# Kernel tuning notes

Hardware: AMD Instinct MI355X
Metric: run time of the kernel (lower is better)

## Reference

```python
import jax, jax.numpy as jnp
import numpy as np

B, LQ, LKV = 32, 512, 512
SIZE, H = 512, 8
HD = SIZE // H
SCALE = 1.0 / np.sqrt(HD)
LN_EPS = 1e-5


def layer_norm(x, w, b):
    mu = jnp.mean(x, axis=-1, keepdims=True)
    var = jnp.mean(jnp.square(x - mu), axis=-1, keepdims=True)
    return (x - mu) * jax.lax.rsqrt(var + LN_EPS) * w + b


def setup_inputs() -> dict:
    key = jax.random.key(0)
    ks = jax.random.split(key, 8)
    s = 0.02
    return {
        "query": jax.random.normal(ks[0], (B, LQ, SIZE), jnp.float32),
        "key_value": jax.random.normal(ks[1], (B, LKV, SIZE), jnp.float32),
        "Wq": jax.random.normal(ks[2], (SIZE, SIZE), jnp.float32) * s,
        "bq": jnp.zeros((SIZE,), jnp.float32),
        "Wk": jax.random.normal(ks[3], (SIZE, SIZE), jnp.float32) * s,
        "bk": jnp.zeros((SIZE,), jnp.float32),
        "Wv": jax.random.normal(ks[4], (SIZE, SIZE), jnp.float32) * s,
        "bv": jnp.zeros((SIZE,), jnp.float32),
        "Wo": jax.random.normal(ks[5], (SIZE, SIZE), jnp.float32) * s,
        "bo": jnp.zeros((SIZE,), jnp.float32),
        "ln0_w": jnp.ones((SIZE,), jnp.float32),
        "ln0_b": jnp.zeros((SIZE,), jnp.float32),
        "ln1_w": jnp.ones((SIZE,), jnp.float32),
        "ln1_b": jnp.zeros((SIZE,), jnp.float32),
    }


def reference(query, key_value, Wq, bq, Wk, bk, Wv, bv, Wo, bo, ln0_w, ln0_b, ln1_w, ln1_b):
    b, lq, _ = query.shape
    lkv = key_value.shape[1]
    # projections
    q = query @ Wq.T + bq          # [B, Lq, SIZE]
    k = key_value @ Wk.T + bk      # [B, Lkv, SIZE]
    v = key_value @ Wv.T + bv
    # split heads: torch cat(split(head_size, 2), 0) == [B,L,H,HD] view with head axis separate
    qh = q.reshape(b, lq, H, HD)
    kh = k.reshape(b, lkv, H, HD)
    vh = v.reshape(b, lkv, H, HD)
    # attention scores [B, H, Lq, Lkv]
    A_ = jnp.einsum("bqhd,bkhd->bhqk", qh, kh) * SCALE
    # signed softmax: tanh(A_) * softmax(sqrt(A_^2 + 0.01)) over keys
    A = jnp.tanh(A_) * jax.nn.softmax(jnp.sqrt(jnp.square(A_) + 0.01), axis=-1)
    # residual q + attention output, merge heads back
    oh = qh + jnp.einsum("bhqk,bkhd->bqhd", A, vh)   # [B, Lq, H, HD]
    output = oh.reshape(b, lq, SIZE)
    output = layer_norm(output, ln0_w, ln0_b)
    output = output + jax.nn.relu(output @ Wo.T + bo)
    output = layer_norm(output, ln1_w, ln1_b)
    return output
```

## Files before the change

kernel.cpp:

```cpp
#include <hip/hip_runtime.h>

#define SIZE_D 512
#define HEADS  8
#define HDIM   64
#define BATCH  32
#define SEQ    512
#define SCALE_F 0.125f
#define NROWS  (BATCH * SEQ)

typedef __attribute__((ext_vector_type(8))) short bf16x8;
typedef __attribute__((ext_vector_type(4))) float f32x4;
typedef __attribute__((ext_vector_type(4))) unsigned int u32x4;

__device__ __forceinline__ unsigned short f2bf(float f) {
    union { float f; unsigned int u; } c{f};
    unsigned int x = c.u;
    x += 0x7fffu + ((x >> 16) & 1u);
    return (unsigned short)(x >> 16);
}

__device__ __forceinline__ void gload_lds16(const unsigned short* g, unsigned short* l) {
    __builtin_amdgcn_global_load_lds(
        (const __attribute__((address_space(1))) unsigned int*)g,
        (__attribute__((address_space(3))) unsigned int*)l, 16, 0, 0);
}

__global__ __launch_bounds__(256) void cvt_bf16(const float* __restrict__ s,
                                                unsigned short* __restrict__ d, int n) {
    const int stride = gridDim.x * blockDim.x * 4;
    for (int i = (blockIdx.x * blockDim.x + threadIdx.x) * 4; i < n; i += stride) {
        const float4 v = *reinterpret_cast<const float4*>(s + i);
        ushort4 o;
        o.x = f2bf(v.x); o.y = f2bf(v.y); o.z = f2bf(v.z); o.w = f2bf(v.w);
        *reinterpret_cast<ushort4*>(d + i) = o;
    }
}

__global__ __launch_bounds__(256) void cvt_w4(const float* __restrict__ w0,
                                              const float* __restrict__ w1,
                                              const float* __restrict__ w2,
                                              const float* __restrict__ w3,
                                              unsigned short* __restrict__ d) {
    const float* srcs[4] = {w0, w1, w2, w3};
    const float* s = srcs[blockIdx.y];
    unsigned short* dst = d + (size_t)blockIdx.y * (SIZE_D * SIZE_D);
    const int n = SIZE_D * SIZE_D;
    const int stride = gridDim.x * blockDim.x * 4;
    for (int i = (blockIdx.x * blockDim.x + threadIdx.x) * 4; i < n; i += stride) {
        const float4 v = *reinterpret_cast<const float4*>(s + i);
        ushort4 o;
        o.x = f2bf(v.x); o.y = f2bf(v.y); o.z = f2bf(v.z); o.w = f2bf(v.w);
        *reinterpret_cast<ushort4*>(dst + i) = o;
    }
}

template <int EPI>
__global__ __launch_bounds__(256, 2) void gemm_mfma(const unsigned short* __restrict__ A,
                                                    const unsigned short* __restrict__ W,
                                                    const float* __restrict__ bias,
                                                    const float* __restrict__ R,
                                                    float* __restrict__ C,
                                                    unsigned short* __restrict__ Hd) {
    __shared__ __align__(16) unsigned short Ad[2][128 * 64];
    __shared__ __align__(16) unsigned short Bd[2][128 * 64];

    const int tid  = threadIdx.x;
    const int wv   = tid >> 6;
    const int lane = tid & 63;
    const int bm   = blockIdx.x * 128;
    const int bn   = blockIdx.y * 128;
    const int wr   = wv >> 1;
    const int wc   = wv & 1;

    auto stage = [&](int buf, int t) {
        const int k0 = t * 64;
#pragma unroll
        for (int i = 0; i < 4; ++i) {
            const int o     = (wv * 32 + i * 8) * 128 + lane * 16;
            const int row   = o >> 7;
            const int inrow = (o & 127) ^ ((row & 7) << 4);
            const int col   = inrow >> 1;
            gload_lds16(A + (size_t)(bm + row) * SIZE_D + k0 + col, &Ad[buf][o >> 1]);
            gload_lds16(W + (size_t)(bn + row) * SIZE_D + k0 + col, &Bd[buf][o >> 1]);
        }
    };

    f32x4 acc[4][4];
#pragma unroll
    for (int mt = 0; mt < 4; ++mt)
#pragma unroll
        for (int nt = 0; nt < 4; ++nt) acc[mt][nt] = (f32x4){0.f, 0.f, 0.f, 0.f};

    stage(0, 0);
    __syncthreads();
    int cur = 0;

    for (int t = 0; t < 8; ++t) {
        if (t < 7) stage(cur ^ 1, t + 1);

        bf16x8 af[2][4], bfr[2][4];
#pragma unroll
        for (int kc = 0; kc < 2; ++kc) {
#pragma unroll
            for (int mt = 0; mt < 4; ++mt) {
                const int r = wr * 64 + mt * 16 + (lane & 15);
                int byte = r * 128 + kc * 64 + (lane >> 4) * 16;
                byte ^= (r & 7) << 4;
                af[kc][mt] = *reinterpret_cast<const bf16x8*>(
                    reinterpret_cast<const char*>(&Ad[cur][0]) + byte);
            }
#pragma unroll
            for (int nt = 0; nt < 4; ++nt) {
                const int r = wc * 64 + nt * 16 + (lane & 15);
                int byte = r * 128 + kc * 64 + (lane >> 4) * 16;
                byte ^= (r & 7) << 4;
                bfr[kc][nt] = *reinterpret_cast<const bf16x8*>(
                    reinterpret_cast<const char*>(&Bd[cur][0]) + byte);
            }
        }
#pragma unroll
        for (int kc = 0; kc < 2; ++kc)
#pragma unroll
            for (int mt = 0; mt < 4; ++mt)
#pragma unroll
                for (int nt = 0; nt < 4; ++nt)
                    acc[mt][nt] = __builtin_amdgcn_mfma_f32_16x16x32_bf16(
                        af[kc][mt], bfr[kc][nt], acc[mt][nt], 0, 0, 0);

        __syncthreads();
        cur ^= 1;
    }

#pragma unroll
    for (int nt = 0; nt < 4; ++nt) {
        const int col  = bn + wc * 64 + nt * 16 + (lane & 15);
        const float bc = bias[col];
#pragma unroll
        for (int mt = 0; mt < 4; ++mt) {
            const int row0 = bm + wr * 64 + mt * 16 + (lane >> 4) * 4;
#pragma unroll
            for (int r = 0; r < 4; ++r) {
                const int row = row0 + r;
                float z = acc[mt][nt][r] + bc;
                if (EPI == 2) {
                    z = R[(size_t)row * SIZE_D + col] + fmaxf(z, 0.0f);
                }
                if (EPI == 1) {
                    const int b_ = row >> 9, l = row & 511;
                    const int h  = col >> 6, dd = col & 63;
                    Hd[(((size_t)b_ * HEADS + h) * SEQ + l) * HDIM + dd] = f2bf(z);
                } else {
                    C[(size_t)row * SIZE_D + col] = z;
                }
            }
        }
    }
}

__global__ __launch_bounds__(512, 2) void attn_mfma(float* __restrict__ q,
                                                    const unsigned short* __restrict__ Kh,
                                                    const unsigned short* __restrict__ Vh) {
    __shared__ __align__(16) unsigned short VtL[64 * 512];
    __shared__ __align__(16) unsigned short WL[8][64 * 64];

    const int tid  = threadIdx.x;
    const int wv   = tid >> 6;
    const int lane = tid & 63;
    const int bh   = blockIdx.x;
    const int b    = bh >> 3;
    const int h    = bh & 7;

    const unsigned short* Kb = Kh + (size_t)bh * (SEQ * HDIM);
    const unsigned short* Vb = Vh + (size_t)bh * (SEQ * HDIM);
    float* qb = q + (size_t)b * (SEQ * SIZE_D) + h * HDIM;

    unsigned short* Tb = &WL[0][0];
    for (int c = 0; c < 8; ++c) {
        {
            const int kv = tid >> 3;
            const int d8 = (tid & 7) * 8;
            u32x4 rv = *reinterpret_cast<const u32x4*>(Vb + (size_t)(c * 64 + kv) * HDIM + d8);
            const unsigned short* rs = reinterpret_cast<const unsigned short*>(&rv);
            __syncthreads();
            unsigned short* dst = &Tb[kv * 66 + d8];
#pragma unroll
            for (int j = 0; j < 8; ++j) dst[j] = rs[j];
        }
        __syncthreads();
        {
            const int d  = tid >> 3;
            const int k8 = (tid & 7) * 8;
            unsigned short tmp[8];
#pragma unroll
            for (int j = 0; j < 8; ++j) tmp[j] = Tb[(k8 + j) * 66 + d];
            int byte = d * 1024 + (c * 64 + k8) * 2;
            byte ^= (d & 7) << 4;
            *reinterpret_cast<u32x4*>(reinterpret_cast<char*>(VtL) + byte) =
                *reinterpret_cast<const u32x4*>(tmp);
        }
    }
    __syncthreads();

    const int m0 = wv * 64;
    bf16x8 qf[4][2];
#pragma unroll
    for (int mt = 0; mt < 4; ++mt)
#pragma unroll
        for (int kc = 0; kc < 2; ++kc) {
            const int m = m0 + mt * 16 + (lane & 15);
            const int d = kc * 32 + (lane >> 4) * 8;
            const float* src = qb + (size_t)m * SIZE_D + d;
            const float4 a0 = *reinterpret_cast<const float4*>(src);
            const float4 a1 = *reinterpret_cast<const float4*>(src + 4);
            union { bf16x8 v; unsigned short s[8]; } u;
            u.s[0] = f2bf(a0.x * SCALE_F); u.s[1] = f2bf(a0.y * SCALE_F);
            u.s[2] = f2bf(a0.z * SCALE_F); u.s[3] = f2bf(a0.w * SCALE_F);
            u.s[4] = f2bf(a1.x * SCALE_F); u.s[5] = f2bf(a1.y * SCALE_F);
            u.s[6] = f2bf(a1.z * SCALE_F); u.s[7] = f2bf(a1.w * SCALE_F);
            qf[mt][kc] = u.v;
        }

    unsigned short* myW = &WL[wv][0];
    f32x4 oacc[4][4];
    float esum[4] = {0.f, 0.f, 0.f, 0.f};
#pragma unroll
    for (int mt = 0; mt < 4; ++mt)
#pragma unroll
        for (int x = 0; x < 4; ++x) oacc[mt][x] = (f32x4){0.f, 0.f, 0.f, 0.f};

    for (int t = 0; t < 8; ++t) {
        const int kv0 = t * 64;
        f32x4 sacc[4][4];
#pragma unroll
        for (int nt = 0; nt < 4; ++nt)
#pragma unroll
            for (int mt = 0; mt < 4; ++mt) sacc[nt][mt] = (f32x4){0.f, 0.f, 0.f, 0.f};

#pragma unroll
        for (int kc = 0; kc < 2; ++kc) {
            bf16x8 kf[4];
#pragma unroll
            for (int nt = 0; nt < 4; ++nt) {
                const int kv = kv0 + nt * 16 + (lane & 15);
                const int d  = kc * 32 + (lane >> 4) * 8;
                union { u32x4 u; bf16x8 v; } cv;
                cv.u = *reinterpret_cast<const u32x4*>(Kb + (size_t)kv * HDIM + d);
                kf[nt] = cv.v;
            }
#pragma unroll
            for (int nt = 0; nt < 4; ++nt)
#pragma unroll
                for (int mt = 0; mt < 4; ++mt)
                    sacc[nt][mt] = __builtin_amdgcn_mfma_f32_16x16x32_bf16(
                        kf[nt], qf[mt][kc], sacc[nt][mt], 0, 0, 0);
        }

#pragma unroll
        for (int nt = 0; nt < 4; ++nt)
#pragma unroll
            for (int mt = 0; mt < 4; ++mt) {
                float w[4];
#pragma unroll
                for (int r = 0; r < 4; ++r) {
                    const float s  = sacc[nt][mt][r];
                    const float tt = __expf(fminf(s + s, 50.0f));
                    const float u  = __builtin_amdgcn_sqrtf(fmaf(s, s, 0.01f));
                    const float ee = __expf(u);
                    esum[mt] += ee;
                    w[r] = (tt - 1.0f) * ee * __builtin_amdgcn_rcpf(tt + 1.0f);
                }
                uint2 pk;
                pk.x = (__float_as_uint(w[1]) & 0xffff0000u) | (__float_as_uint(w[0]) >> 16);
                pk.y = (__float_as_uint(w[3]) & 0xffff0000u) | (__float_as_uint(w[2]) >> 16);
                int byte = (mt * 16 + (lane & 15)) * 128 + nt * 32 + (lane >> 4) * 8;
                byte ^= (lane & 7) << 4;
                *reinterpret_cast<uint2*>(reinterpret_cast<char*>(myW) + byte) = pk;
            }

#pragma unroll
        for (int kc2 = 0; kc2 < 2; ++kc2) {
            bf16x8 wf[4], vf[4];
#pragma unroll
            for (int mt = 0; mt < 4; ++mt) {
                const int row = mt * 16 + (lane & 15);
                int byte = row * 128 + kc2 * 64 + (lane >> 4) * 16;
                byte ^= (row & 7) << 4;
                union { u32x4 u; bf16x8 v; } cv;
                cv.u = *reinterpret_cast<const u32x4*>(reinterpret_cast<char*>(myW) + byte);
                wf[mt] = cv.v;
            }
#pragma unroll
            for (int dt = 0; dt < 4; ++dt) {
                const int d = dt * 16 + (lane & 15);
                int byte = d * 1024 + (kv0 + kc2 * 32 + (lane >> 4) * 8) * 2;
                byte ^= (d & 7) << 4;
                union { u32x4 u; bf16x8 v; } cv;
                cv.u = *reinterpret_cast<const u32x4*>(reinterpret_cast<char*>(VtL) + byte);
                vf[dt] = cv.v;
            }
#pragma unroll
            for (int mt = 0; mt < 4; ++mt)
#pragma unroll
                for (int dt = 0; dt < 4; ++dt)
                    oacc[mt][dt] = __builtin_amdgcn_mfma_f32_16x16x32_bf16(
                        wf[mt], vf[dt], oacc[mt][dt], 0, 0, 0);
        }
    }

    float rden[4];
#pragma unroll
    for (int mt = 0; mt < 4; ++mt) {
        float e = esum[mt];
        e += __shfl_xor(e, 16);
        e += __shfl_xor(e, 32);
        rden[mt] = __builtin_amdgcn_rcpf(e);
    }
    float rr_[4][4];
#pragma unroll
    for (int mt = 0; mt < 4; ++mt)
#pragma unroll
        for (int r = 0; r < 4; ++r)
            rr_[mt][r] = __shfl(rden[mt], (lane >> 4) * 4 + r);

#pragma unroll
    for (int mt = 0; mt < 4; ++mt)
#pragma unroll
        for (int dt = 0; dt < 4; ++dt)
#pragma unroll
            for (int r = 0; r < 4; ++r) {
                const int m = m0 + mt * 16 + (lane >> 4) * 4 + r;
                const int d = dt * 16 + (lane & 15);
                float* p = qb + (size_t)m * SIZE_D + d;
                *p = *p + oacc[mt][dt][r] * rr_[mt][r];
            }
}

template <int BF16OUT>
__global__ __launch_bounds__(256) void ln_kernel(const float* __restrict__ in,
                                                 const float* __restrict__ w,
                                                 const float* __restrict__ b,
                                                 float* __restrict__ out,
                                                 unsigned short* __restrict__ outb) {
    const int row = blockIdx.x;
    const int tid = threadIdx.x;
    const float2 x = *reinterpret_cast<const float2*>(&in[(size_t)row * SIZE_D + tid * 2]);

    float s  = x.x + x.y;
    float sq = x.x * x.x + x.y * x.y;
#pragma unroll
    for (int off = 32; off > 0; off >>= 1) {
        s  += __shfl_xor(s, off);
        sq += __shfl_xor(sq, off);
    }
    __shared__ float rs[4], rq[4];
    const int wv = tid >> 6;
    if ((tid & 63) == 0) { rs[wv] = s; rq[wv] = sq; }
    __syncthreads();
    s  = rs[0] + rs[1] + rs[2] + rs[3];
    sq = rq[0] + rq[1] + rq[2] + rq[3];

    const float mu  = s * (1.0f / SIZE_D);
    const float var = sq * (1.0f / SIZE_D) - mu * mu;
    const float rr  = rsqrtf(var + 1e-5f);

    const float2 wv2 = *reinterpret_cast<const float2*>(&w[tid * 2]);
    const float2 bv2 = *reinterpret_cast<const float2*>(&b[tid * 2]);
    float2 o;
    o.x = (x.x - mu) * rr * wv2.x + bv2.x;
    o.y = (x.y - mu) * rr * wv2.y + bv2.y;
    *reinterpret_cast<float2*>(&out[(size_t)row * SIZE_D + tid * 2]) = o;
    if (BF16OUT) {
        ushort2 ob;
        ob.x = f2bf(o.x); ob.y = f2bf(o.y);
        *reinterpret_cast<ushort2*>(&outb[(size_t)row * SIZE_D + tid * 2]) = ob;
    }
}

extern "C" void kernel_launch(void* const* d_in, const int* in_sizes, int n_in,
                              void* d_out, int out_size, void* d_ws, size_t ws_size,
                              hipStream_t stream) {
    const float* query = (const float*)d_in[0];
    const float* keyv  = (const float*)d_in[1];
    const float* Wq    = (const float*)d_in[2];
    const float* bq    = (const float*)d_in[3];
    const float* Wk    = (const float*)d_in[4];
    const float* bk    = (const float*)d_in[5];
    const float* Wv    = (const float*)d_in[6];
    const float* bv    = (const float*)d_in[7];
    const float* Wo    = (const float*)d_in[8];
    const float* bo    = (const float*)d_in[9];
    const float* ln0w  = (const float*)d_in[10];
    const float* ln0b  = (const float*)d_in[11];
    const float* ln1w  = (const float*)d_in[12];
    const float* ln1b  = (const float*)d_in[13];
    float* out = (float*)d_out;

    char* ws = (char*)d_ws;
    float*          qbuf = (float*)ws;
    unsigned short* Kh   = (unsigned short*)(ws + ((size_t)32 << 20));
    unsigned short* Vh   = (unsigned short*)(ws + ((size_t)48 << 20));
    float*          obuf = (float*)(ws + ((size_t)32 << 20));
    unsigned short* Qbf  = (unsigned short*)(ws + ((size_t)64 << 20));
    unsigned short* KVbf = (unsigned short*)(ws + ((size_t)80 << 20));
    unsigned short* Xbf  = KVbf;

    unsigned short* Wbf = (unsigned short*)d_out;
    unsigned short* WqB = Wbf;
    unsigned short* WkB = Wbf + 262144;
    unsigned short* WvB = Wbf + 524288;
    unsigned short* WoB = Wbf + 786432;

    const int NACT = NROWS * SIZE_D;

    cvt_bf16<<<2048, 256, 0, stream>>>(query, Qbf, NACT);
    cvt_bf16<<<2048, 256, 0, stream>>>(keyv, KVbf, NACT);
    cvt_w4<<<dim3(64, 4), 256, 0, stream>>>(Wq, Wk, Wv, Wo, Wbf);

    const dim3 gg(NROWS / 128, SIZE_D / 128);

    gemm_mfma<0><<<gg, 256, 0, stream>>>(Qbf,  WqB, bq, nullptr, qbuf, nullptr);
    gemm_mfma<1><<<gg, 256, 0, stream>>>(KVbf, WkB, bk, nullptr, nullptr, Kh);
    gemm_mfma<1><<<gg, 256, 0, stream>>>(KVbf, WvB, bv, nullptr, nullptr, Vh);

    attn_mfma<<<BATCH * HEADS, 512, 0, stream>>>(qbuf, Kh, Vh);

    ln_kernel<1><<<NROWS, 256, 0, stream>>>(qbuf, ln0w, ln0b, qbuf, Xbf);
    gemm_mfma<2><<<gg, 256, 0, stream>>>(Xbf, WoB, bo, qbuf, obuf, nullptr);
    ln_kernel<0><<<NROWS, 256, 0, stream>>>(obuf, ln1w, ln1b, out, nullptr);
}
```

Baseline: 180.8 us.

## Fuse K/V projections, store bf16 head-major Q, fuse output projection with LayerNorm

Restructures most of the pipeline. The two activation conversions become one launch. K and V are computed in a single N=1024 GEMM, with the attention scale folded into K and V written pre-transposed. Q is stored as bf16 in head-major layout. Attention reads V straight from global memory and splits each head's queries across two blocks. The output projection is fused with ReLU, the residual and the final LayerNorm, and the tanh/exp math is reformulated to share one exponential. This removes the in-kernel V transpose, fp32 intermediate traffic and a separate LayerNorm pass. The cost is that the residuals now use bf16-rounded values, which lowers precision.

```diff
diff --git a/kernel.cpp b/kernel.cpp
--- a/kernel.cpp
+++ b/kernel.cpp
@@ -18,15 +18,24 @@
     x += 0x7fffu + ((x >> 16) & 1u);
     return (unsigned short)(x >> 16);
 }
-
+__device__ __forceinline__ float bf2f(unsigned short u) {
+    union { unsigned int i; float f; } c;
+    c.i = (unsigned int)u << 16;
+    return c.f;
+}
 __device__ __forceinline__ void gload_lds16(const unsigned short* g, unsigned short* l) {
     __builtin_amdgcn_global_load_lds(
         (const __attribute__((address_space(1))) unsigned int*)g,
         (__attribute__((address_space(3))) unsigned int*)l, 16, 0, 0);
 }
 
-__global__ __launch_bounds__(256) void cvt_bf16(const float* __restrict__ s,
-                                                unsigned short* __restrict__ d, int n) {
+__global__ __launch_bounds__(256) void cvt_act(const float* __restrict__ q,
+                                               const float* __restrict__ kv,
+                                               unsigned short* __restrict__ dq,
+                                               unsigned short* __restrict__ dkv) {
+    const float* s = blockIdx.y ? kv : q;
+    unsigned short* d = blockIdx.y ? dkv : dq;
+    const int n = NROWS * SIZE_D;
     const int stride = gridDim.x * blockDim.x * 4;
     for (int i = (blockIdx.x * blockDim.x + threadIdx.x) * 4; i < n; i += stride) {
         const float4 v = *reinterpret_cast<const float4*>(s + i);
@@ -54,13 +63,13 @@
     }
 }
 
-template <int EPI>
-__global__ __launch_bounds__(256, 2) void gemm_mfma(const unsigned short* __restrict__ A,
+template <int KV>
+__global__ __launch_bounds__(256, 2) void gemm_proj(const unsigned short* __restrict__ A,
                                                     const unsigned short* __restrict__ W,
-                                                    const float* __restrict__ bias,
-                                                    const float* __restrict__ R,
-                                                    float* __restrict__ C,
-                                                    unsigned short* __restrict__ Hd) {
+                                                    const float* __restrict__ bias0,
+                                                    const float* __restrict__ bias1,
+                                                    unsigned short* __restrict__ D0,
+                                                    unsigned short* __restrict__ D1) {
     __shared__ __align__(16) unsigned short Ad[2][128 * 64];
     __shared__ __align__(16) unsigned short Bd[2][128 * 64];
 
@@ -131,93 +140,77 @@
         cur ^= 1;
     }
 
-#pragma unroll
-    for (int nt = 0; nt < 4; ++nt) {
-        const int col  = bn + wc * 64 + nt * 16 + (lane & 15);
-        const float bc = bias[col];
-#pragma unroll
-        for (int mt = 0; mt < 4; ++mt) {
-            const int row0 = bm + wr * 64 + mt * 16 + (lane >> 4) * 4;
-#pragma unroll
-            for (int r = 0; r < 4; ++r) {
-                const int row = row0 + r;
-                float z = acc[mt][nt][r] + bc;
-                if (EPI == 2) {
-                    z = R[(size_t)row * SIZE_D + col] + fmaxf(z, 0.0f);
+    if (KV == 0 || bn < 512) {
+#pragma unroll
+        for (int nt = 0; nt < 4; ++nt) {
+            const int col = bn + wc * 64 + nt * 16 + (lane & 15);
+            const float bc = bias0[col];
+            const int h = (col >> 6) & 7, dd = col & 63;
+#pragma unroll
+            for (int mt = 0; mt < 4; ++mt) {
+                const int row0 = bm + wr * 64 + mt * 16 + (lane >> 4) * 4;
+#pragma unroll
+                for (int r = 0; r < 4; ++r) {
+                    const int row = row0 + r;
+                    const int b_ = row >> 9, l = row & 511;
+                    float z = acc[mt][nt][r] + bc;
+                    if (KV) z *= SCALE_F;
+                    D0[(((size_t)b_ * HEADS + h) * SEQ + l) * HDIM + dd] = f2bf(z);
                 }
-                if (EPI == 1) {
-                    const int b_ = row >> 9, l = row & 511;
-                    const int h  = col >> 6, dd = col & 63;
-                    Hd[(((size_t)b_ * HEADS + h) * SEQ + l) * HDIM + dd] = f2bf(z);
-                } else {
-                    C[(size_t)row * SIZE_D + col] = z;
-                }
-            }
-        }
-    }
-}
-
-__global__ __launch_bounds__(512, 2) void attn_mfma(float* __restrict__ q,
+            }
+        }
+    } else {
+#pragma unroll
+        for (int nt = 0; nt < 4; ++nt) {
+            const int c2 = bn + wc * 64 + nt * 16 + (lane & 15) - 512;
+            const float bc = bias1[c2];
+            const int hV = c2 >> 6, dV = c2 & 63;
+#pragma unroll
+            for (int mt = 0; mt < 4; ++mt) {
+                const int row0 = bm + wr * 64 + mt * 16 + (lane >> 4) * 4;
+                const int b_ = row0 >> 9, kv = row0 & 511;
+                ushort4 pk;
+                pk.x = f2bf(acc[mt][nt][0] + bc);
+                pk.y = f2bf(acc[mt][nt][1] + bc);
+                pk.z = f2bf(acc[mt][nt][2] + bc);
+                pk.w = f2bf(acc[mt][nt][3] + bc);
+                *reinterpret_cast<ushort4*>(
+                    &D1[(((size_t)b_ * HEADS + hV) * HDIM + dV) * SEQ + kv]) = pk;
+            }
+        }
+    }
+}
+
+__global__ __launch_bounds__(256, 2) void attn_mfma(const unsigned short* __restrict__ Qh,
                                                     const unsigned short* __restrict__ Kh,
-                                                    const unsigned short* __restrict__ Vh) {
-    __shared__ __align__(16) unsigned short VtL[64 * 512];
-    __shared__ __align__(16) unsigned short WL[8][64 * 64];
+                                                    const unsigned short* __restrict__ Vt,
+                                                    float* __restrict__ outq) {
+    __shared__ __align__(16) unsigned short WL[4][64 * 64];
 
     const int tid  = threadIdx.x;
     const int wv   = tid >> 6;
     const int lane = tid & 63;
     const int bh   = blockIdx.x;
+    const int half = blockIdx.y;
     const int b    = bh >> 3;
     const int h    = bh & 7;
 
+    const unsigned short* Qb = Qh + (size_t)bh * (SEQ * HDIM);
     const unsigned short* Kb = Kh + (size_t)bh * (SEQ * HDIM);
-    const unsigned short* Vb = Vh + (size_t)bh * (SEQ * HDIM);
-    float* qb = q + (size_t)b * (SEQ * SIZE_D) + h * HDIM;
-
-    unsigned short* Tb = &WL[0][0];
-    for (int c = 0; c < 8; ++c) {
-        {
-            const int kv = tid >> 3;
-            const int d8 = (tid & 7) * 8;
-            u32x4 rv = *reinterpret_cast<const u32x4*>(Vb + (size_t)(c * 64 + kv) * HDIM + d8);
-            const unsigned short* rs = reinterpret_cast<const unsigned short*>(&rv);
-            __syncthreads();
-            unsigned short* dst = &Tb[kv * 66 + d8];
-#pragma unroll
-            for (int j = 0; j < 8; ++j) dst[j] = rs[j];
-        }
-        __syncthreads();
-        {
-            const int d  = tid >> 3;
-            const int k8 = (tid & 7) * 8;
-            unsigned short tmp[8];
-#pragma unroll
-            for (int j = 0; j < 8; ++j) tmp[j] = Tb[(k8 + j) * 66 + d];
-            int byte = d * 1024 + (c * 64 + k8) * 2;
-            byte ^= (d & 7) << 4;
-            *reinterpret_cast<u32x4*>(reinterpret_cast<char*>(VtL) + byte) =
-                *reinterpret_cast<const u32x4*>(tmp);
-        }
-    }
-    __syncthreads();
-
-    const int m0 = wv * 64;
+    const unsigned short* Vb = Vt + (size_t)bh * (HDIM * SEQ);
+
+    const int m0 = half * 256 + wv * 64;
+
     bf16x8 qf[4][2];
 #pragma unroll
     for (int mt = 0; mt < 4; ++mt)
 #pragma unroll
         for (int kc = 0; kc < 2; ++kc) {
             const int m = m0 + mt * 16 + (lane & 15);
-            const int d = kc * 32 + (lane >> 4) * 8;
-            const float* src = qb + (size_t)m * SIZE_D + d;
-            const float4 a0 = *reinterpret_cast<const float4*>(src);
-            const float4 a1 = *reinterpret_cast<const float4*>(src + 4);
-            union { bf16x8 v; unsigned short s[8]; } u;
-            u.s[0] = f2bf(a0.x * SCALE_F); u.s[1] = f2bf(a0.y * SCALE_F);
-            u.s[2] = f2bf(a0.z * SCALE_F); u.s[3] = f2bf(a0.w * SCALE_F);
-            u.s[4] = f2bf(a1.x * SCALE_F); u.s[5] = f2bf(a1.y * SCALE_F);
-            u.s[6] = f2bf(a1.z * SCALE_F); u.s[7] = f2bf(a1.w * SCALE_F);
-            qf[mt][kc] = u.v;
+            union { u32x4 u; bf16x8 v; } cv;
+            cv.u = *reinterpret_cast<const u32x4*>(
+                Qb + (size_t)m * HDIM + kc * 32 + (lane >> 4) * 8);
+            qf[mt][kc] = cv.v;
         }
 
     unsigned short* myW = &WL[wv][0];
@@ -242,9 +235,9 @@
 #pragma unroll
             for (int nt = 0; nt < 4; ++nt) {
                 const int kv = kv0 + nt * 16 + (lane & 15);
-                const int d  = kc * 32 + (lane >> 4) * 8;
                 union { u32x4 u; bf16x8 v; } cv;
-                cv.u = *reinterpret_cast<const u32x4*>(Kb + (size_t)kv * HDIM + d);
+                cv.u = *reinterpret_cast<const u32x4*>(
+                    Kb + (size_t)kv * HDIM + kc * 32 + (lane >> 4) * 8);
                 kf[nt] = cv.v;
             }
 #pragma unroll
@@ -263,11 +256,16 @@
 #pragma unroll
                 for (int r = 0; r < 4; ++r) {
                     const float s  = sacc[nt][mt][r];
-                    const float tt = __expf(fminf(s + s, 50.0f));
+                    const float a  = fminf(fabsf(s), 30.0f);
+                    const float tt = __expf(a);
+                    const float t2 = tt * tt;
                     const float u  = __builtin_amdgcn_sqrtf(fmaf(s, s, 0.01f));
-                    const float ee = __expf(u);
-                    esum[mt] += ee;
-                    w[r] = (tt - 1.0f) * ee * __builtin_amdgcn_rcpf(tt + 1.0f);
+                    const float dl = u - a;
+                    const float ed = fmaf(dl, fmaf(dl, fmaf(dl, 0.16666667f, 0.5f), 1.0f), 1.0f);
+                    const float eu = tt * ed;
+                    esum[mt] += eu;
+                    const float th = (t2 - 1.0f) * __builtin_amdgcn_rcpf(t2 + 1.0f);
+                    w[r] = __builtin_copysignf(th * eu, s);
                 }
                 uint2 pk;
                 pk.x = (__float_as_uint(w[1]) & 0xffff0000u) | (__float_as_uint(w[0]) >> 16);
@@ -292,10 +290,9 @@
 #pragma unroll
             for (int dt = 0; dt < 4; ++dt) {
                 const int d = dt * 16 + (lane & 15);
-                int byte = d * 1024 + (kv0 + kc2 * 32 + (lane >> 4) * 8) * 2;
-                byte ^= (d & 7) << 4;
                 union { u32x4 u; bf16x8 v; } cv;
-                cv.u = *reinterpret_cast<const u32x4*>(reinterpret_cast<char*>(VtL) + byte);
+                cv.u = *reinterpret_cast<const u32x4*>(
+                    Vb + (size_t)d * SEQ + kv0 + kc2 * 32 + (lane >> 4) * 8);
                 vf[dt] = cv.v;
             }
 #pragma unroll
@@ -330,17 +327,16 @@
             for (int r = 0; r < 4; ++r) {
                 const int m = m0 + mt * 16 + (lane >> 4) * 4 + r;
                 const int d = dt * 16 + (lane & 15);
-                float* p = qb + (size_t)m * SIZE_D + d;
-                *p = *p + oacc[mt][dt][r] * rr_[mt][r];
-            }
-}
-
-template <int BF16OUT>
-__global__ __launch_bounds__(256) void ln_kernel(const float* __restrict__ in,
-                                                 const float* __restrict__ w,
-                                                 const float* __restrict__ b,
-                                                 float* __restrict__ out,
-                                                 unsigned short* __restrict__ outb) {
+                const float qv = bf2f(Qb[(size_t)m * HDIM + d]);
+                outq[((size_t)b * SEQ + m) * SIZE_D + h * HDIM + d] =
+                    qv + oacc[mt][dt][r] * rr_[mt][r];
+            }
+}
+
+__global__ __launch_bounds__(256) void ln0_bf16(const float* __restrict__ in,
+                                                const float* __restrict__ w,
+                                                const float* __restrict__ b,
+                                                unsigned short* __restrict__ outb) {
     const int row = blockIdx.x;
     const int tid = threadIdx.x;
     const float2 x = *reinterpret_cast<const float2*>(&in[(size_t)row * SIZE_D + tid * 2]);
@@ -365,14 +361,157 @@
 
     const float2 wv2 = *reinterpret_cast<const float2*>(&w[tid * 2]);
     const float2 bv2 = *reinterpret_cast<const float2*>(&b[tid * 2]);
-    float2 o;
-    o.x = (x.x - mu) * rr * wv2.x + bv2.x;
-    o.y = (x.y - mu) * rr * wv2.y + bv2.y;
-    *reinterpret_cast<float2*>(&out[(size_t)row * SIZE_D + tid * 2]) = o;
-    if (BF16OUT) {
-        ushort2 ob;
-        ob.x = f2bf(o.x); ob.y = f2bf(o.y);
-        *reinterpret_cast<ushort2*>(&outb[(size_t)row * SIZE_D + tid * 2]) = ob;
+    ushort2 ob;
+    ob.x = f2bf((x.x - mu) * rr * wv2.x + bv2.x);
+    ob.y = f2bf((x.y - mu) * rr * wv2.y + bv2.y);
+    *reinterpret_cast<ushort2*>(&outb[(size_t)row * SIZE_D + tid * 2]) = ob;
+}
+
+__global__ __launch_bounds__(512, 2) void oproj_ln(const unsigned short* __restrict__ X,
+                                                   const unsigned short* __restrict__ W,
+                                                   const float* __restrict__ bo,
+                                                   const float* __restrict__ g1,
+                                                   const float* __restrict__ b1,
+                                                   float* __restrict__ out) {
+    __shared__ __align__(16) unsigned short Ad[2][64 * 64];
+    __shared__ __align__(16) unsigned short Bd[2][512 * 64];
+    __shared__ float red[64][8][2];
+    __shared__ float stat[64][2];
+
+    const int tid  = threadIdx.x;
+    const int wv   = tid >> 6;
+    const int lane = tid & 63;
+    const int bm   = blockIdx.x * 64;
+
+    auto stage = [&](int buf, int t) {
+        const int k0 = t * 64;
+        {
+            const int o     = tid * 16;
+            const int row   = o >> 7;
+            const int inrow = (o & 127) ^ ((row & 7) << 4);
+            const int col   = inrow >> 1;
+            gload_lds16(X + (size_t)(bm + row) * SIZE_D + k0 + col, &Ad[buf][o >> 1]);
+        }
+#pragma unroll
+        for (int i = 0; i < 8; ++i) {
+            const int o     = i * 8192 + tid * 16;
+            const int row   = o >> 7;
+            const int inrow = (o & 127) ^ ((row & 7) << 4);
+            const int col   = inrow >> 1;
+            gload_lds16(W + (size_t)row * SIZE_D + k0 + col, &Bd[buf][o >> 1]);
+        }
+    };
+
+    f32x4 acc[4][4];
+#pragma unroll
+    for (int mt = 0; mt < 4; ++mt)
+#pragma unroll
+        for (int nt = 0; nt < 4; ++nt) acc[mt][nt] = (f32x4){0.f, 0.f, 0.f, 0.f};
+
+    stage(0, 0);
+    __syncthreads();
+    int cur = 0;
+
+    for (int t = 0; t < 8; ++t) {
+        if (t < 7) stage(cur ^ 1, t + 1);
+
+        bf16x8 af[2][4], bfr[2][4];
+#pragma unroll
+        for (int kc = 0; kc < 2; ++kc) {
+#pragma unroll
+            for (int mt = 0; mt < 4; ++mt) {
+                const int r = mt * 16 + (lane & 15);
+                int byte = r * 128 + kc * 64 + (lane >> 4) * 16;
+                byte ^= (r & 7) << 4;
+                af[kc][mt] = *reinterpret_cast<const bf16x8*>(
+                    reinterpret_cast<const char*>(&Ad[cur][0]) + byte);
+            }
+#pragma unroll
+            for (int nt = 0; nt < 4; ++nt) {
+                const int r = wv * 64 + nt * 16 + (lane & 15);
+                int byte = r * 128 + kc * 64 + (lane >> 4) * 16;
+                byte ^= (r & 7) << 4;
+                bfr[kc][nt] = *reinterpret_cast<const bf16x8*>(
+                    reinterpret_cast<const char*>(&Bd[cur][0]) + byte);
+            }
+        }
+#pragma unroll
+        for (int kc = 0; kc < 2; ++kc)
+#pragma unroll
+            for (int mt = 0; mt < 4; ++mt)
+#pragma unroll
+                for (int nt = 0; nt < 4; ++nt)
+                    acc[mt][nt] = __builtin_amdgcn_mfma_f32_16x16x32_bf16(
+                        af[kc][mt], bfr[kc][nt], acc[mt][nt], 0, 0, 0);
+
+        __syncthreads();
+        cur ^= 1;
+    }
+
+#pragma unroll
+    for (int nt = 0; nt < 4; ++nt) {
+        const int n  = wv * 64 + nt * 16 + (lane & 15);
+        const float bc = bo[n];
+#pragma unroll
+        for (int mt = 0; mt < 4; ++mt) {
+            const int row0 = bm + mt * 16 + (lane >> 4) * 4;
+#pragma unroll
+            for (int r = 0; r < 4; ++r) {
+                const float R = bf2f(X[(size_t)(row0 + r) * SIZE_D + n]);
+                acc[mt][nt][r] = R + fmaxf(acc[mt][nt][r] + bc, 0.0f);
+            }
+        }
+    }
+
+    float ps[4][4], pq[4][4];
+#pragma unroll
+    for (int mt = 0; mt < 4; ++mt)
+#pragma unroll
+        for (int r = 0; r < 4; ++r) {
+            float s = 0.f, q = 0.f;
+#pragma unroll
+            for (int nt = 0; nt < 4; ++nt) {
+                const float v = acc[mt][nt][r];
+                s += v; q += v * v;
+            }
+#pragma unroll
+            for (int off = 1; off <= 8; off <<= 1) {
+                s += __shfl_xor(s, off);
+                q += __shfl_xor(q, off);
+            }
+            ps[mt][r] = s; pq[mt][r] = q;
+        }
+    {
+        const int mtw = (lane & 15) >> 2, rw = lane & 3;
+        const int rowL = mtw * 16 + (lane >> 4) * 4 + rw;
+        red[rowL][wv][0] = ps[mtw][rw];
+        red[rowL][wv][1] = pq[mtw][rw];
+    }
+    __syncthreads();
+    if (tid < 64) {
+        float s = 0.f, q = 0.f;
+#pragma unroll
+        for (int w8 = 0; w8 < 8; ++w8) { s += red[tid][w8][0]; q += red[tid][w8][1]; }
+        const float mu  = s * (1.0f / SIZE_D);
+        const float var = q * (1.0f / SIZE_D) - mu * mu;
+        stat[tid][0] = mu;
+        stat[tid][1] = rsqrtf(var + 1e-5f);
+    }
+    __syncthreads();
+
+#pragma unroll
+    for (int nt = 0; nt < 4; ++nt) {
+        const int n = wv * 64 + nt * 16 + (lane & 15);
+        const float g = g1[n], bb = b1[n];
+#pragma unroll
+        for (int mt = 0; mt < 4; ++mt) {
+#pragma unroll
+            for (int r = 0; r < 4; ++r) {
+                const int rowL = mt * 16 + (lane >> 4) * 4 + r;
+                const float y = (acc[mt][nt][r] - stat[rowL][0]) * stat[rowL][1];
+                out[(size_t)(bm + rowL) * SIZE_D + n] = y * g + bb;
+            }
+        }
     }
 }
 
@@ -396,35 +535,27 @@
     float* out = (float*)d_out;
 
     char* ws = (char*)d_ws;
+    unsigned short* Qbf  = (unsigned short*)ws;
+    unsigned short* KVbf = (unsigned short*)(ws + ((size_t)16 << 20));
     float*          qbuf = (float*)ws;
-    unsigned short* Kh   = (unsigned short*)(ws + ((size_t)32 << 20));
-    unsigned short* Vh   = (unsigned short*)(ws + ((size_t)48 << 20));
-    float*          obuf = (float*)(ws + ((size_t)32 << 20));
-    unsigned short* Qbf  = (unsigned short*)(ws + ((size_t)64 << 20));
-    unsigned short* KVbf = (unsigned short*)(ws + ((size_t)80 << 20));
-    unsigned short* Xbf  = KVbf;
-
-    unsigned short* Wbf = (unsigned short*)d_out;
-    unsigned short* WqB = Wbf;
-    unsigned short* WkB = Wbf + 262144;
-    unsigned short* WvB = Wbf + 524288;
-    unsigned short* WoB = Wbf + 786432;
-
-    const int NACT = NROWS * SIZE_D;
-
-    cvt_bf16<<<2048, 256, 0, stream>>>(query, Qbf, NACT);
-    cvt_bf16<<<2048, 256, 0, stream>>>(keyv, KVbf, NACT);
+    unsigned short* Qh   = (unsigned short*)(ws + ((size_t)32 << 20));
+    unsigned short* Xbf  = Qh;
+    unsigned short* Kh   = (unsigned short*)(ws + ((size_t)48 << 20));
+    unsigned short* Vt   = (unsigned short*)(ws + ((size_t)64 << 20));
+    unsigned short* Wbf  = (unsigned short*)(ws + ((size_t)80 << 20));
+    unsigned short* WqB  = Wbf;
+    unsigned short* WkB  = Wbf + 262144;
+    unsigned short* WoB  = Wbf + 786432;
+
+    cvt_act<<<dim3(1024, 2), 256, 0, stream>>>(query, keyv, Qbf, KVbf);
     cvt_w4<<<dim3(64, 4), 256, 0, stream>>>(Wq, Wk, Wv, Wo, Wbf);
 
-    const dim3 gg(NROWS / 128, SIZE_D / 128);
-
-    gemm_mfma<0><<<gg, 256, 0, stream>>>(Qbf,  WqB, bq, nullptr, qbuf, nullptr);
-    gemm_mfma<1><<<gg, 256, 0, stream>>>(KVbf, WkB, bk, nullptr, nullptr, Kh);
-    gemm_mfma<1><<<gg, 256, 0, stream>>>(KVbf, WvB, bv, nullptr, nullptr, Vh);
-
-    attn_mfma<<<BATCH * HEADS, 512, 0, stream>>>(qbuf, Kh, Vh);
-
-    ln_kernel<1><<<NROWS, 256, 0, stream>>>(qbuf, ln0w, ln0b, qbuf, Xbf);
-    gemm_mfma<2><<<gg, 256, 0, stream>>>(Xbf, WoB, bo, qbuf, obuf, nullptr);
-    ln_kernel<0><<<NROWS, 256, 0, stream>>>(obuf, ln1w, ln1b, out, nullptr);
-}
+    gemm_proj<0><<<dim3(128, 4), 256, 0, stream>>>(Qbf, WqB, bq, nullptr, Qh, nullptr);
+    gemm_proj<1><<<dim3(128, 8), 256, 0, stream>>>(KVbf, WkB, bk, bv, Kh, Vt);
+
+    attn_mfma<<<dim3(BATCH * HEADS, 2), 256, 0, stream>>>(Qh, Kh, Vt, qbuf);
+
+    ln0_bf16<<<NROWS, 256, 0, stream>>>(qbuf, ln0w, ln0b, Xbf);
+
+    oproj_ln<<<NROWS / 64, 512, 0, stream>>>(Xbf, WoB, bo, ln1w, ln1b, out);
+}
```

Measured after the change: 171.7 us. -5.0%, faster.
